# Kernel tuning notes

Hardware: AMD Instinct MI355X
Metric: run time of the kernel (lower is better)

Reference implementation:

```python
import jax, jax.numpy as jnp
import numpy as np

B, T, C = 4, 2048, 2048
H = 16
D = C // H  # 128


def setup_inputs() -> dict:
    key = jax.random.key(0)
    ks = jax.random.split(key, 9)
    s = 0.02
    return {
        "x": jax.random.normal(ks[0], (B, T, C), dtype=jnp.float32),
        "wq": jax.random.normal(ks[1], (C, C), dtype=jnp.float32) * s,
        "bq": jax.random.normal(ks[2], (C,), dtype=jnp.float32) * s,
        "wk": jax.random.normal(ks[3], (C, C), dtype=jnp.float32) * s,
        "bk": jax.random.normal(ks[4], (C,), dtype=jnp.float32) * s,
        "wv": jax.random.normal(ks[5], (C, C), dtype=jnp.float32) * s,
        "bv": jax.random.normal(ks[6], (C,), dtype=jnp.float32) * s,
        "wo": jax.random.normal(ks[7], (C, C), dtype=jnp.float32) * s,
        "bo": jax.random.normal(ks[8], (C,), dtype=jnp.float32) * s,
    }


def reference(x, wq, bq, wk, bk, wv, bv, wo, bo):
    Bz, Tz, Cz = x.shape
    # projections (torch Linear: x @ W^T + b)
    q = (x @ wq.T + bq).reshape(Bz, Tz, H, D).transpose(0, 2, 1, 3)  # [B,H,T,D]
    k = (x @ wk.T + bk).reshape(Bz, Tz, H, D).transpose(0, 2, 1, 3)
    v = (x @ wv.T + bv).reshape(Bz, Tz, H, D).transpose(0, 2, 1, 3)
    scale = 1.0 / jnp.sqrt(jnp.float32(D))
    scores = jnp.einsum("bhqd,bhkd->bhqk", q, k) * scale  # [B,H,T,T]
    causal = jnp.tril(jnp.ones((Tz, Tz), dtype=bool))
    scores = jnp.where(causal, scores, jnp.float32(-jnp.inf))
    att = jax.nn.softmax(scores, axis=-1)
    out = jnp.einsum("bhqk,bhkd->bhqd", att, v)  # [B,H,T,D]
    out = out.transpose(0, 2, 1, 3).reshape(Bz, Tz, Cz)
    out = out @ wo.T + bo
    return out
```

## Files before the change

### kernel.cpp

```cpp
#include <hip/hip_runtime.h>
#include <hip/hip_bf16.h>

typedef float  f32x4  __attribute__((ext_vector_type(4)));
typedef __bf16 bf16x8 __attribute__((ext_vector_type(8)));
typedef __bf16 bf16x4 __attribute__((ext_vector_type(4)));

#define Bz 4
#define Tz 2048
#define Cz 2048
#define Hh 16
#define Dd 128
#define Mm 8192

__device__ __forceinline__ void gload_lds16(const __bf16* g, __bf16* l) {
  __builtin_amdgcn_global_load_lds(
      (const __attribute__((address_space(1))) void*)g,
      (__attribute__((address_space(3))) void*)l, 16, 0, 0);
}

__global__ __launch_bounds__(256)
void cvt_bf16(const float* __restrict__ in, __bf16* __restrict__ out, int n8) {
  int i = blockIdx.x * 256 + threadIdx.x;
  if (i >= n8) return;
  size_t base = (size_t)i * 8;
  f32x4 a = *(const f32x4*)(in + base);
  f32x4 b = *(const f32x4*)(in + base + 4);
  bf16x8 o;
  o[0]=(__bf16)a[0]; o[1]=(__bf16)a[1]; o[2]=(__bf16)a[2]; o[3]=(__bf16)a[3];
  o[4]=(__bf16)b[0]; o[5]=(__bf16)b[1]; o[6]=(__bf16)b[2]; o[7]=(__bf16)b[3];
  *(bf16x8*)(out + base) = o;
}

template<int MODE>
__global__ __launch_bounds__(256, 2)
void gemm_bt(const __bf16* __restrict__ A, const __bf16* __restrict__ W,
             const float* __restrict__ bias, void* __restrict__ Out,
             int K, float scale)
{
  __shared__ __bf16 As[128 * 64];
  __shared__ __bf16 Bs[128 * 64];

  const int tid  = threadIdx.x;
  const int lane = tid & 63;
  const int wave = tid >> 6;
  const int wm = wave >> 1, wn = wave & 1;
  const int g  = lane >> 4;
  const int lr = lane & 15;
  const int row0 = blockIdx.x * 128;
  const int col0 = blockIdx.y * 128;

  const int srow = lane >> 3;
  const int sblk = lane & 7;

  f32x4 acc[4][4] = {};

  for (int kt = 0; kt < K; kt += 64) {
    __syncthreads();
    #pragma unroll
    for (int p = 0; p < 4; ++p) {
      const int rb = p * 32 + wave * 8;
      const int r  = rb + srow;
      const int cb = sblk ^ (r & 7);
      gload_lds16(A + (size_t)(row0 + r) * K + kt + cb * 8, As + rb * 64);
      gload_lds16(W + (size_t)(col0 + r) * K + kt + cb * 8, Bs + rb * 64);
    }
    __syncthreads();
    #pragma unroll
    for (int kk = 0; kk < 2; ++kk) {
      bf16x8 af[4], bfr[4];
      #pragma unroll
      for (int i = 0; i < 4; ++i) {
        const int ar = wm * 64 + i * 16 + lr;
        af[i]  = *(const bf16x8*)(As + ar * 64 + ((((kk<<2)|g) ^ (ar & 7)) << 3));
        const int br = wn * 64 + i * 16 + lr;
        bfr[i] = *(const bf16x8*)(Bs + br * 64 + ((((kk<<2)|g) ^ (br & 7)) << 3));
      }
      #pragma unroll
      for (int i = 0; i < 4; ++i)
        #pragma unroll
        for (int j = 0; j < 4; ++j)
          acc[i][j] = __builtin_amdgcn_mfma_f32_16x16x32_bf16(af[i], bfr[j], acc[i][j], 0, 0, 0);
    }
  }

  #pragma unroll
  for (int j = 0; j < 4; ++j) {
    const int col = col0 + wn * 64 + j * 16 + lr;
    const float bv = bias[col];
    #pragma unroll
    for (int i = 0; i < 4; ++i) {
      if (MODE == 2) {
        const int row = row0 + wm * 64 + i * 16 + g * 4;
        const int b = row >> 11, t = row & (Tz - 1);
        const int h = col >> 7,  d = col & (Dd - 1);
        bf16x4 v4;
        #pragma unroll
        for (int r = 0; r < 4; ++r) v4[r] = (__bf16)(acc[i][j][r] + bv);
        *(bf16x4*)((__bf16*)Out + ((size_t)(b * Hh + h) * Dd + d) * Tz + t) = v4;
      } else {
        #pragma unroll
        for (int r = 0; r < 4; ++r) {
          const int row = row0 + wm * 64 + i * 16 + g * 4 + r;
          const float v = acc[i][j][r] + bv;
          if (MODE == 0) {
            const int b = row >> 11, t = row & (Tz - 1);
            const int h = col >> 7,  d = col & (Dd - 1);
            ((__bf16*)Out)[((size_t)(b * Hh + h) * Tz + t) * Dd + d] = (__bf16)(v * scale);
          } else {
            ((float*)Out)[(size_t)row * Cz + col] = v;
          }
        }
      }
    }
  }
}

__global__ __launch_bounds__(256, 2)
void attn_fwd(const __bf16* __restrict__ Q, const __bf16* __restrict__ Kg,
              const __bf16* __restrict__ Vt, __bf16* __restrict__ O)
{
  __shared__ __bf16 Ks[64 * 128];
  __shared__ __bf16 Vs[128 * 64];
  __shared__ __bf16 Ps[4][32 * 72];

  const int tid  = threadIdx.x;
  const int lane = tid & 63;
  const int wave = tid >> 6;
  const int g  = lane >> 4;
  const int lr = lane & 15;
  const int pair = blockIdx.y;
  const int b = pair >> 4, h = pair & 15;

  const __bf16* Qp = Q  + (size_t)pair * Tz * Dd;
  const __bf16* Kp = Kg + (size_t)pair * Tz * Dd;
  const __bf16* Vp = Vt + (size_t)pair * Dd * Tz;

  const int krow[4] = { 0*16 + wave*4 + (lane>>4), 1*16 + wave*4 + (lane>>4),
                        2*16 + wave*4 + (lane>>4), 3*16 + wave*4 + (lane>>4) };
  const int vrow[4] = { 0*32 + wave*8 + (lane>>3), 1*32 + wave*8 + (lane>>3),
                        2*32 + wave*8 + (lane>>3), 3*32 + wave*8 + (lane>>3) };

  #pragma unroll
  for (int pass = 0; pass < 2; ++pass) {
    const int qt  = pass == 0 ? (15 - blockIdx.x) : blockIdx.x;
    const int qw0 = qt * 128 + wave * 32;

    bf16x8 qf[2][4];
    #pragma unroll
    for (int im = 0; im < 2; ++im)
      #pragma unroll
      for (int ks = 0; ks < 4; ++ks)
        qf[im][ks] = *(const bf16x8*)(Qp + (size_t)(qw0 + im*16 + lr) * Dd + ks*32 + g*8);

    f32x4 oacc[2][8] = {};
    float mrow[2][4], lsum[2][4];
    #pragma unroll
    for (int im = 0; im < 2; ++im)
      #pragma unroll
      for (int r = 0; r < 4; ++r) { mrow[im][r] = -1e30f; lsum[im][r] = 0.f; }

    const int ntiles = 2 * qt + 2;
    for (int kt = 0; kt < ntiles; ++kt) {
      const int kv0 = kt * 64;
      __syncthreads();
      #pragma unroll
      for (int p = 0; p < 4; ++p) {
        const int r  = krow[p];
        const int cb = (lane & 15) ^ (r & 7);
        gload_lds16(Kp + (size_t)(kv0 + r) * Dd + cb * 8, Ks + p * 2048 + wave * 512);
        const int d  = vrow[p];
        const int cv = (lane & 7) ^ (d & 7);
        gload_lds16(Vp + (size_t)d * Tz + kv0 + cv * 8, Vs + p * 2048 + wave * 512);
      }
      __syncthreads();

      if (kv0 <= qw0 + 31) {
        f32x4 sacc[2][4] = {};
        #pragma unroll
        for (int ks = 0; ks < 4; ++ks) {
          bf16x8 kf[4];
          #pragma unroll
          for (int in = 0; in < 4; ++in) {
            const int r = in*16 + lr;
            kf[in] = *(const bf16x8*)(Ks + r * 128 + ((((ks<<2)|g) ^ (r & 7)) << 3));
          }
          #pragma unroll
          for (int im = 0; im < 2; ++im)
            #pragma unroll
            for (int in = 0; in < 4; ++in)
              sacc[im][in] = __builtin_amdgcn_mfma_f32_16x16x32_bf16(qf[im][ks], kf[in], sacc[im][in], 0, 0, 0);
        }
        if (kv0 + 63 > qw0) {
          #pragma unroll
          for (int im = 0; im < 2; ++im)
            #pragma unroll
            for (int in = 0; in < 4; ++in)
              #pragma unroll
              for (int r = 0; r < 4; ++r) {
                const int qrow = qw0 + im*16 + g*4 + r;
                const int kcol = kv0 + in*16 + lr;
                if (kcol > qrow) sacc[im][in][r] = -3e38f;
              }
        }
        #pragma unroll
        for (int im = 0; im < 2; ++im) {
          float mx[4], corr[4];
          #pragma unroll
          for (int r = 0; r < 4; ++r) {
            float m = fmaxf(fmaxf(sacc[im][0][r], sacc[im][1][r]),
                            fmaxf(sacc[im][2][r], sacc[im][3][r]));
            #pragma unroll
            for (int off = 1; off < 16; off <<= 1)
              m = fmaxf(m, __shfl_xor(m, off));
            const float mn = fmaxf(mrow[im][r], m);
            corr[r] = __expf(mrow[im][r] - mn);
            mrow[im][r] = mn;
            mx[r] = mn;
          }
          float rs[4] = {0.f, 0.f, 0.f, 0.f};
          #pragma unroll
          for (int in = 0; in < 4; ++in) {
            #pragma unroll
            for (int r = 0; r < 4; ++r) {
              const float pv = __expf(sacc[im][in][r] - mx[r]);
              rs[r] += pv;
              Ps[wave][(im*16 + g*4 + r) * 72 + in*16 + lr] = (__bf16)pv;
            }
          }
          #pragma unroll
          for (int r = 0; r < 4; ++r) {
            float s = rs[r];
            #pragma unroll
            for (int off = 1; off < 16; off <<= 1)
              s += __shfl_xor(s, off);
            lsum[im][r] = lsum[im][r] * corr[r] + s;
            #pragma unroll
            for (int dn = 0; dn < 8; ++dn)
              oacc[im][dn][r] *= corr[r];
          }
        }
        #pragma unroll
        for (int kk = 0; kk < 2; ++kk) {
          bf16x8 pa[2];
          #pragma unroll
          for (int im = 0; im < 2; ++im)
            pa[im] = *(const bf16x8*)(&Ps[wave][(im*16 + lr) * 72 + kk*32 + g*8]);
          #pragma unroll
          for (int dn = 0; dn < 8; ++dn) {
            const int d = dn*16 + lr;
            bf16x8 vb = *(const bf16x8*)(Vs + d * 64 + ((((kk<<2)|g) ^ (d & 7)) << 3));
            #pragma unroll
            for (int im = 0; im < 2; ++im)
              oacc[im][dn] = __builtin_amdgcn_mfma_f32_16x16x32_bf16(pa[im], vb, oacc[im][dn], 0, 0, 0);
          }
        }
      }
    }

    #pragma unroll
    for (int im = 0; im < 2; ++im)
      #pragma unroll
      for (int dn = 0; dn < 8; ++dn)
        #pragma unroll
        for (int r = 0; r < 4; ++r) {
          const int qrow = qw0 + im*16 + g*4 + r;
          const float v = oacc[im][dn][r] / lsum[im][r];
          O[((size_t)(b * Tz + qrow)) * Cz + h * Dd + dn*16 + lr] = (__bf16)v;
        }
  }
}

extern "C" void kernel_launch(void* const* d_in, const int* in_sizes, int n_in,
                              void* d_out, int out_size, void* d_ws, size_t ws_size,
                              hipStream_t stream) {
  const float* x  = (const float*)d_in[0];
  const float* wq = (const float*)d_in[1];
  const float* bq = (const float*)d_in[2];
  const float* wk = (const float*)d_in[3];
  const float* bk = (const float*)d_in[4];
  const float* wv = (const float*)d_in[5];
  const float* bv = (const float*)d_in[6];
  const float* wo = (const float*)d_in[7];
  const float* bo = (const float*)d_in[8];
  float* out = (float*)d_out;

  char* w = (char*)d_ws;
  __bf16* xb   = (__bf16*)w; w += (size_t)Mm * Cz * 2;
  __bf16* wbuf = (__bf16*)w; w += (size_t)Cz * Cz * 2;
  __bf16* qb   = (__bf16*)w; w += (size_t)Mm * Cz * 2;
  __bf16* kb   = (__bf16*)w; w += (size_t)Mm * Cz * 2;
  __bf16* vbuf = (__bf16*)w; w += (size_t)Mm * Cz * 2;
  if (ws_size < (size_t)(w - (char*)d_ws)) return;

  const int nx8 = Mm * Cz / 8;
  const int nw8 = Cz * Cz / 8;
  dim3 ggrid(Mm / 128, Cz / 128);
  const float qscale = 0.08838834764831845f;

  cvt_bf16<<<nx8 / 256, 256, 0, stream>>>(x, xb, nx8);

  cvt_bf16<<<nw8 / 256, 256, 0, stream>>>(wq, wbuf, nw8);
  gemm_bt<0><<<ggrid, 256, 0, stream>>>(xb, wbuf, bq, qb, Cz, qscale);

  cvt_bf16<<<nw8 / 256, 256, 0, stream>>>(wk, wbuf, nw8);
  gemm_bt<0><<<ggrid, 256, 0, stream>>>(xb, wbuf, bk, kb, Cz, 1.0f);

  cvt_bf16<<<nw8 / 256, 256, 0, stream>>>(wv, wbuf, nw8);
  gemm_bt<2><<<ggrid, 256, 0, stream>>>(xb, wbuf, bv, vbuf, Cz, 1.0f);

  __bf16* ob = xb;
  attn_fwd<<<dim3(8, Bz * Hh), 256, 0, stream>>>(qb, kb, vbuf, ob);

  cvt_bf16<<<nw8 / 256, 256, 0, stream>>>(wo, wbuf, nw8);
  gemm_bt<1><<<ggrid, 256, 0, stream>>>(ob, wbuf, bo, out, Cz, 1.0f);
}
```

Before: 465.1 us.

## Double-buffer K/V tiles in attention and use lazy exp2 softmax rescaling

Adds double-buffered K/V shared-memory staging so the next tile's async global-to-LDS loads overlap the current tile's compute, with one barrier per iteration instead of two. Folds log2(e) into the Q scale so softmax uses the hardware exp2, and rescales the running max and accumulators only when the new max exceeds the old one by a threshold. Also XOR-swizzles the P buffer instead of padding it and raises wave priority around the MFMA sections. This roughly doubles K/V LDS use, which may reduce occupancy, and the lazy rescale relies on fp32 headroom for the deferred maximum.

```diff
diff --git a/kernel.cpp b/kernel.cpp
--- a/kernel.cpp
+++ b/kernel.cpp
@@ -119,9 +119,9 @@
 void attn_fwd(const __bf16* __restrict__ Q, const __bf16* __restrict__ Kg,
               const __bf16* __restrict__ Vt, __bf16* __restrict__ O)
 {
-  __shared__ __bf16 Ks[64 * 128];
-  __shared__ __bf16 Vs[128 * 64];
-  __shared__ __bf16 Ps[4][32 * 72];
+  __shared__ __bf16 Ks[2][64 * 128];
+  __shared__ __bf16 Vs[2][128 * 64];
+  __shared__ __bf16 Ps[4][32 * 64];
 
   const int tid  = threadIdx.x;
   const int lane = tid & 63;
@@ -135,14 +135,24 @@
   const __bf16* Kp = Kg + (size_t)pair * Tz * Dd;
   const __bf16* Vp = Vt + (size_t)pair * Dd * Tz;
 
-  const int krow[4] = { 0*16 + wave*4 + (lane>>4), 1*16 + wave*4 + (lane>>4),
-                        2*16 + wave*4 + (lane>>4), 3*16 + wave*4 + (lane>>4) };
-  const int vrow[4] = { 0*32 + wave*8 + (lane>>3), 1*32 + wave*8 + (lane>>3),
-                        2*32 + wave*8 + (lane>>3), 3*32 + wave*8 + (lane>>3) };
-
-  #pragma unroll
+  #define STAGE_KV(kv0_, buf_)                                                  \
+    {                                                                           \
+      const int kv0s = (kv0_);                                                  \
+      _Pragma("unroll")                                                         \
+      for (int p = 0; p < 4; ++p) {                                             \
+        const int r  = p * 16 + wave * 4 + (lane >> 4);                         \
+        const int cb = (lane & 15) ^ (r & 7);                                   \
+        gload_lds16(Kp + (size_t)(kv0s + r) * Dd + cb * 8,                      \
+                    &Ks[buf_][p * 2048 + wave * 512]);                          \
+        const int d  = p * 32 + wave * 8 + (lane >> 3);                         \
+        const int cv = (lane & 7) ^ (d & 7);                                    \
+        gload_lds16(Vp + (size_t)d * Tz + kv0s + cv * 8,                        \
+                    &Vs[buf_][p * 2048 + wave * 512]);                          \
+      }                                                                         \
+    }
+
   for (int pass = 0; pass < 2; ++pass) {
-    const int qt  = pass == 0 ? (15 - blockIdx.x) : blockIdx.x;
+    const int qt  = pass == 0 ? (15 - (int)blockIdx.x) : (int)blockIdx.x;
     const int qw0 = qt * 128 + wave * 32;
 
     bf16x8 qf[2][4];
@@ -160,29 +170,25 @@
       for (int r = 0; r < 4; ++r) { mrow[im][r] = -1e30f; lsum[im][r] = 0.f; }
 
     const int ntiles = 2 * qt + 2;
+
+    STAGE_KV(0, 0);
+    __syncthreads();
+
     for (int kt = 0; kt < ntiles; ++kt) {
+      const int cur = kt & 1;
       const int kv0 = kt * 64;
-      __syncthreads();
-      #pragma unroll
-      for (int p = 0; p < 4; ++p) {
-        const int r  = krow[p];
-        const int cb = (lane & 15) ^ (r & 7);
-        gload_lds16(Kp + (size_t)(kv0 + r) * Dd + cb * 8, Ks + p * 2048 + wave * 512);
-        const int d  = vrow[p];
-        const int cv = (lane & 7) ^ (d & 7);
-        gload_lds16(Vp + (size_t)d * Tz + kv0 + cv * 8, Vs + p * 2048 + wave * 512);
-      }
-      __syncthreads();
+      if (kt + 1 < ntiles) STAGE_KV((kt + 1) * 64, cur ^ 1);
 
       if (kv0 <= qw0 + 31) {
         f32x4 sacc[2][4] = {};
+        __builtin_amdgcn_s_setprio(1);
         #pragma unroll
         for (int ks = 0; ks < 4; ++ks) {
           bf16x8 kf[4];
           #pragma unroll
           for (int in = 0; in < 4; ++in) {
             const int r = in*16 + lr;
-            kf[in] = *(const bf16x8*)(Ks + r * 128 + ((((ks<<2)|g) ^ (r & 7)) << 3));
+            kf[in] = *(const bf16x8*)(&Ks[cur][r * 128 + ((((ks<<2)|g) ^ (r & 7)) << 3)]);
           }
           #pragma unroll
           for (int im = 0; im < 2; ++im)
@@ -190,6 +196,7 @@
             for (int in = 0; in < 4; ++in)
               sacc[im][in] = __builtin_amdgcn_mfma_f32_16x16x32_bf16(qf[im][ks], kf[in], sacc[im][in], 0, 0, 0);
         }
+        __builtin_amdgcn_s_setprio(0);
         if (kv0 + 63 > qw0) {
           #pragma unroll
           for (int im = 0; im < 2; ++im)
@@ -204,7 +211,7 @@
         }
         #pragma unroll
         for (int im = 0; im < 2; ++im) {
-          float mx[4], corr[4];
+          float pmax[4];
           #pragma unroll
           for (int r = 0; r < 4; ++r) {
             float m = fmaxf(fmaxf(sacc[im][0][r], sacc[im][1][r]),
@@ -212,19 +219,34 @@
             #pragma unroll
             for (int off = 1; off < 16; off <<= 1)
               m = fmaxf(m, __shfl_xor(m, off));
-            const float mn = fmaxf(mrow[im][r], m);
-            corr[r] = __expf(mrow[im][r] - mn);
-            mrow[im][r] = mn;
-            mx[r] = mn;
+            pmax[r] = m;
+          }
+          bool need = false;
+          #pragma unroll
+          for (int r = 0; r < 4; ++r) need |= (pmax[r] > mrow[im][r] + 11.54f);
+          if (__any(need)) {
+            #pragma unroll
+            for (int r = 0; r < 4; ++r) {
+              const bool  up = pmax[r] > mrow[im][r] + 11.54f;
+              const float mn = up ? pmax[r] : mrow[im][r];
+              const float corr = exp2f(mrow[im][r] - mn);
+              mrow[im][r] = mn;
+              lsum[im][r] *= corr;
+              #pragma unroll
+              for (int dn = 0; dn < 8; ++dn)
+                oacc[im][dn][r] *= corr;
+            }
           }
           float rs[4] = {0.f, 0.f, 0.f, 0.f};
           #pragma unroll
           for (int in = 0; in < 4; ++in) {
             #pragma unroll
             for (int r = 0; r < 4; ++r) {
-              const float pv = __expf(sacc[im][in][r] - mx[r]);
+              const float pv = __builtin_amdgcn_exp2f(sacc[im][in][r] - mrow[im][r]);
               rs[r] += pv;
-              Ps[wave][(im*16 + g*4 + r) * 72 + in*16 + lr] = (__bf16)pv;
+              const int row = im*16 + g*4 + r;
+              const int col = in*16 + lr;
+              Ps[wave][row * 64 + ((((col >> 3) ^ (row & 7)) << 3) | (col & 7))] = (__bf16)pv;
             }
           }
           #pragma unroll
@@ -233,28 +255,30 @@
             #pragma unroll
             for (int off = 1; off < 16; off <<= 1)
               s += __shfl_xor(s, off);
-            lsum[im][r] = lsum[im][r] * corr[r] + s;
-            #pragma unroll
-            for (int dn = 0; dn < 8; ++dn)
-              oacc[im][dn][r] *= corr[r];
-          }
-        }
+            lsum[im][r] += s;
+          }
+        }
+        __builtin_amdgcn_s_setprio(1);
         #pragma unroll
         for (int kk = 0; kk < 2; ++kk) {
           bf16x8 pa[2];
           #pragma unroll
-          for (int im = 0; im < 2; ++im)
-            pa[im] = *(const bf16x8*)(&Ps[wave][(im*16 + lr) * 72 + kk*32 + g*8]);
+          for (int im = 0; im < 2; ++im) {
+            const int row = im*16 + lr;
+            pa[im] = *(const bf16x8*)(&Ps[wave][row * 64 + ((((kk<<2)|g) ^ (row & 7)) << 3)]);
+          }
           #pragma unroll
           for (int dn = 0; dn < 8; ++dn) {
             const int d = dn*16 + lr;
-            bf16x8 vb = *(const bf16x8*)(Vs + d * 64 + ((((kk<<2)|g) ^ (d & 7)) << 3));
+            bf16x8 vb = *(const bf16x8*)(&Vs[cur][d * 64 + ((((kk<<2)|g) ^ (d & 7)) << 3)]);
             #pragma unroll
             for (int im = 0; im < 2; ++im)
               oacc[im][dn] = __builtin_amdgcn_mfma_f32_16x16x32_bf16(pa[im], vb, oacc[im][dn], 0, 0, 0);
           }
         }
+        __builtin_amdgcn_s_setprio(0);
       }
+      __syncthreads();
     }
 
     #pragma unroll
@@ -268,6 +292,7 @@
           O[((size_t)(b * Tz + qrow)) * Cz + h * Dd + dn*16 + lr] = (__bf16)v;
         }
   }
+  #undef STAGE_KV
 }
 
 extern "C" void kernel_launch(void* const* d_in, const int* in_sizes, int n_in,
@@ -295,7 +320,7 @@
   const int nx8 = Mm * Cz / 8;
   const int nw8 = Cz * Cz / 8;
   dim3 ggrid(Mm / 128, Cz / 128);
-  const float qscale = 0.08838834764831845f;
+  const float qscale = 0.12752551286084110f;
 
   cvt_bf16<<<nx8 / 256, 256, 0, stream>>>(x, xb, nx8);
 
```

Measured after the change: 454.0 us. -2.4%, faster.
